# Kernel optimization log

Measured on AMD Instinct MI355X. Metric: run time of the kernel, lower is better.

The kernel has to match this reference:

```python
import jax, jax.numpy as jnp
import numpy as np

RESOLUTION = 128


def _bin_mask():
    # [4, 2] bool: corner i, dim d -> True if corner uses floor coord in dim d
    neigs = jnp.arange(4, dtype=jnp.int32)[:, None]
    dims = jnp.arange(2, dtype=jnp.int32)[None, :]
    return (neigs & (1 << dims)) == 0


def setup_inputs() -> dict:
    key = jax.random.key(0)
    k1, k2 = jax.random.split(key)
    batch = 65536
    res, map_num, feat_dim = RESOLUTION, 128, 8
    inputs = jax.random.uniform(k1, (batch, 2), dtype=jnp.float32)
    # xavier_uniform over [res^2, map_num*feat_dim]
    fan_in, fan_out = res * res, map_num * feat_dim
    bound = float(np.sqrt(6.0 / (fan_in + fan_out)))
    embeddings = jax.random.uniform(k2, (res * res, map_num * feat_dim),
                                    dtype=jnp.float32, minval=-bound, maxval=bound)
    return {"inputs": inputs, "embeddings": embeddings}


def reference(inputs, embeddings):
    res = RESOLUTION
    bin_mask = _bin_mask()                      # [4, 2]
    x = inputs * (res - 1)                      # [B, 2]
    xi = jnp.floor(x).astype(jnp.int32)         # [B, 2]
    xf = x - jax.lax.stop_gradient(jnp.floor(x))  # fractional part, grads flow via x
    xi = xi[:, None, :]                         # [B, 1, 2]
    xf = xf[:, None, :]                         # [B, 1, 2]
    neigs = jnp.where(bin_mask, xi, xi + 1)     # [B, 4, 2]
    ids = neigs[..., 0] * res + neigs[..., 1]   # [B, 4]
    neigs_features = embeddings[ids]            # [B, 4, D] irregular gather
    weights = jnp.where(bin_mask, 1.0 - xf, xf) # [B, 4, 2]
    w = jnp.prod(weights, axis=-1, keepdims=True)  # [B, 4, 1]
    return jnp.sum(neigs_features * w, axis=-2)    # [B, D]
```

## Files before the change

kernel.cpp:

```cpp
#include <hip/hip_runtime.h>

#define RES   128
#define FEAT  1024
#define NBINS (RES * RES)

__global__ __launch_bounds__(256)
void hist_kernel(const float* __restrict__ inputs, unsigned* __restrict__ hist, int N)
{
    int p = blockIdx.x * 256 + threadIdx.x;
    if (p >= N) return;
    int i0 = (int)floorf(inputs[2 * p + 0] * (float)(RES - 1));
    int i1 = (int)floorf(inputs[2 * p + 1] * (float)(RES - 1));
    atomicAdd(&hist[i0 * RES + i1], 1u);
}

__global__ __launch_bounds__(256)
void scan_kernel(unsigned* __restrict__ hist)
{
    __shared__ unsigned part[256];
    int t = threadIdx.x;
    int base = t * 64;
    unsigned s = 0;
    for (int k = 0; k < 64; ++k) s += hist[base + k];
    part[t] = s;
    __syncthreads();
    if (t == 0) {
        unsigned run = 0;
        for (int i = 0; i < 256; ++i) { unsigned v = part[i]; part[i] = run; run += v; }
    }
    __syncthreads();
    unsigned run = part[t];
    for (int k = 0; k < 64; ++k) { unsigned v = hist[base + k]; hist[base + k] = run; run += v; }
}

__global__ __launch_bounds__(256)
void scatter_kernel(const float* __restrict__ inputs, unsigned* __restrict__ hist,
                    unsigned* __restrict__ order, int N)
{
    int p = blockIdx.x * 256 + threadIdx.x;
    if (p >= N) return;
    int i0 = (int)floorf(inputs[2 * p + 0] * (float)(RES - 1));
    int i1 = (int)floorf(inputs[2 * p + 1] * (float)(RES - 1));
    unsigned pos = atomicAdd(&hist[i0 * RES + i1], 1u);
    order[pos] = (unsigned)p;
}

__global__ __launch_bounds__(256)
void DenseMap_sorted_kernel(const float* __restrict__ inputs,
                            const float* __restrict__ emb,
                            const unsigned* __restrict__ order,
                            float* __restrict__ out,
                            int N, int chunk)
{
    const int b = blockIdx.x;
    const int c = threadIdx.x;
    const int g = (chunk > 0) ? ((b & 7) * chunk + (b >> 3)) : b;

#pragma unroll
    for (int j = 0; j < 4; ++j) {
        const int s = g * 4 + j;
        if (s >= N) break;
        const int p = (int)order[s];

        const float x0 = inputs[2 * p + 0] * (float)(RES - 1);
        const float x1 = inputs[2 * p + 1] * (float)(RES - 1);
        const float f0 = floorf(x0);
        const float f1 = floorf(x1);
        const int   i0 = (int)f0;
        const int   i1 = (int)f1;
        const float xf0 = x0 - f0;
        const float xf1 = x1 - f1;

        const float w00 = (1.0f - xf0) * (1.0f - xf1);
        const float w01 = (1.0f - xf0) * xf1;
        const float w10 = xf0 * (1.0f - xf1);
        const float w11 = xf0 * xf1;

        const long base = (long)(i0 * RES + i1) * FEAT;
        const float4 a = ((const float4*)(emb + base))[c];
        const float4 bb = ((const float4*)(emb + base + FEAT))[c];
        const float4 gg = ((const float4*)(emb + base + (long)RES * FEAT))[c];
        const float4 h = ((const float4*)(emb + base + (long)RES * FEAT + FEAT))[c];

        float4 r;
        r.x = a.x * w00 + bb.x * w01 + gg.x * w10 + h.x * w11;
        r.y = a.y * w00 + bb.y * w01 + gg.y * w10 + h.y * w11;
        r.z = a.z * w00 + bb.z * w01 + gg.z * w10 + h.z * w11;
        r.w = a.w * w00 + bb.w * w01 + gg.w * w10 + h.w * w11;

        ((float4*)(out + (long)p * FEAT))[c] = r;
    }
}

__global__ __launch_bounds__(256)
void DenseMap_fallback_kernel(const float* __restrict__ inputs,
                              const float* __restrict__ emb,
                              float* __restrict__ out)
{
    const int p = blockIdx.x;
    const int c = threadIdx.x;

    const float x0 = inputs[2 * p + 0] * (float)(RES - 1);
    const float x1 = inputs[2 * p + 1] * (float)(RES - 1);
    const float f0 = floorf(x0);
    const float f1 = floorf(x1);
    const int   i0 = (int)f0;
    const int   i1 = (int)f1;
    const float xf0 = x0 - f0;
    const float xf1 = x1 - f1;

    const float w00 = (1.0f - xf0) * (1.0f - xf1);
    const float w01 = (1.0f - xf0) * xf1;
    const float w10 = xf0 * (1.0f - xf1);
    const float w11 = xf0 * xf1;

    const long base = (long)(i0 * RES + i1) * FEAT;
    const float4 a = ((const float4*)(emb + base))[c];
    const float4 b = ((const float4*)(emb + base + FEAT))[c];
    const float4 g = ((const float4*)(emb + base + (long)RES * FEAT))[c];
    const float4 h = ((const float4*)(emb + base + (long)RES * FEAT + FEAT))[c];

    float4 r;
    r.x = a.x * w00 + b.x * w01 + g.x * w10 + h.x * w11;
    r.y = a.y * w00 + b.y * w01 + g.y * w10 + h.y * w11;
    r.z = a.z * w00 + b.z * w01 + g.z * w10 + h.z * w11;
    r.w = a.w * w00 + b.w * w01 + g.w * w10 + h.w * w11;

    ((float4*)(out + (long)p * FEAT))[c] = r;
}

extern "C" void kernel_launch(void* const* d_in, const int* in_sizes, int n_in,
                              void* d_out, int out_size, void* d_ws, size_t ws_size,
                              hipStream_t stream)
{
    const float* inputs = (const float*)d_in[0];
    const float* emb    = (const float*)d_in[1];
    float*       out    = (float*)d_out;

    const int N = in_sizes[0] / 2;
    const size_t need = (size_t)(NBINS + N) * sizeof(unsigned);

    if (ws_size >= need) {
        unsigned* hist  = (unsigned*)d_ws;
        unsigned* order = hist + NBINS;

        hipMemsetAsync(hist, 0, NBINS * sizeof(unsigned), stream);
        hist_kernel<<<(N + 255) / 256, 256, 0, stream>>>(inputs, hist, N);
        scan_kernel<<<1, 256, 0, stream>>>(hist);
        scatter_kernel<<<(N + 255) / 256, 256, 0, stream>>>(inputs, hist, order, N);

        const int G = (N + 3) / 4;
        const int chunk = (G % 8 == 0) ? (G / 8) : 0;
        DenseMap_sorted_kernel<<<G, 256, 0, stream>>>(inputs, emb, order, out, N, chunk);
    } else {
        DenseMap_fallback_kernel<<<N, 256, 0, stream>>>(inputs, emb, out);
    }
}
```

Baseline: 389.2 us.

## Process one grid cell per block, reusing corner embeddings across its points

Replaces the per-point sorted kernel with a per-cell kernel that loads the four corner embedding rows once and applies them to every point falling in that cell. Point indices and coordinates are staged through shared memory, and outputs use nontemporal stores. This removes redundant embedding reads across points sharing a cell. It adds barriers per batch and can leave blocks with uneven amounts of work.

Measured after the change: 347.7 us. -10.7%, faster.

```diff
diff --git a/kernel.cpp b/kernel.cpp
--- a/kernel.cpp
+++ b/kernel.cpp
@@ -4,13 +4,16 @@
 #define FEAT  1024
 #define NBINS (RES * RES)
 
+typedef float nfloat4 __attribute__((ext_vector_type(4)));
+
 __global__ __launch_bounds__(256)
 void hist_kernel(const float* __restrict__ inputs, unsigned* __restrict__ hist, int N)
 {
     int p = blockIdx.x * 256 + threadIdx.x;
     if (p >= N) return;
-    int i0 = (int)floorf(inputs[2 * p + 0] * (float)(RES - 1));
-    int i1 = (int)floorf(inputs[2 * p + 1] * (float)(RES - 1));
+    const float2 uv = ((const float2*)inputs)[p];
+    int i0 = (int)floorf(uv.x * (float)(RES - 1));
+    int i1 = (int)floorf(uv.y * (float)(RES - 1));
     atomicAdd(&hist[i0 * RES + i1], 1u);
 }
 
@@ -39,56 +42,73 @@
 {
     int p = blockIdx.x * 256 + threadIdx.x;
     if (p >= N) return;
-    int i0 = (int)floorf(inputs[2 * p + 0] * (float)(RES - 1));
-    int i1 = (int)floorf(inputs[2 * p + 1] * (float)(RES - 1));
+    const float2 uv = ((const float2*)inputs)[p];
+    int i0 = (int)floorf(uv.x * (float)(RES - 1));
+    int i1 = (int)floorf(uv.y * (float)(RES - 1));
     unsigned pos = atomicAdd(&hist[i0 * RES + i1], 1u);
     order[pos] = (unsigned)p;
 }
 
 __global__ __launch_bounds__(256)
-void DenseMap_sorted_kernel(const float* __restrict__ inputs,
-                            const float* __restrict__ emb,
-                            const unsigned* __restrict__ order,
-                            float* __restrict__ out,
-                            int N, int chunk)
+void DenseMap_cell_kernel(const float* __restrict__ inputs,
+                          const float* __restrict__ emb,
+                          const unsigned* __restrict__ hist,
+                          const unsigned* __restrict__ order,
+                          float* __restrict__ out,
+                          int chunk)
 {
-    const int b = blockIdx.x;
-    const int c = threadIdx.x;
-    const int g = (chunk > 0) ? ((b & 7) * chunk + (b >> 3)) : b;
+    const int b    = blockIdx.x;
+    const int cell = (chunk > 0) ? ((b & 7) * chunk + (b >> 3)) : b;
+    const int c    = threadIdx.x;
 
-#pragma unroll
-    for (int j = 0; j < 4; ++j) {
-        const int s = g * 4 + j;
-        if (s >= N) break;
-        const int p = (int)order[s];
+    const unsigned start = (cell == 0) ? 0u : hist[cell - 1];
+    const unsigned end   = hist[cell];
+    if (start == end) return;
 
-        const float x0 = inputs[2 * p + 0] * (float)(RES - 1);
-        const float x1 = inputs[2 * p + 1] * (float)(RES - 1);
-        const float f0 = floorf(x0);
-        const float f1 = floorf(x1);
-        const int   i0 = (int)f0;
-        const int   i1 = (int)f1;
-        const float xf0 = x0 - f0;
-        const float xf1 = x1 - f1;
+    const int i0 = cell >> 7;
+    const int i1 = cell & (RES - 1);
 
-        const float w00 = (1.0f - xf0) * (1.0f - xf1);
-        const float w01 = (1.0f - xf0) * xf1;
-        const float w10 = xf0 * (1.0f - xf1);
-        const float w11 = xf0 * xf1;
+    const long base = (long)cell * FEAT;
+    const float4 r00 = ((const float4*)(emb + base))[c];
+    const float4 r01 = ((const float4*)(emb + base + FEAT))[c];
+    const float4 r10 = ((const float4*)(emb + base + (long)RES * FEAT))[c];
+    const float4 r11 = ((const float4*)(emb + base + (long)RES * FEAT + FEAT))[c];
 
-        const long base = (long)(i0 * RES + i1) * FEAT;
-        const float4 a = ((const float4*)(emb + base))[c];
-        const float4 bb = ((const float4*)(emb + base + FEAT))[c];
-        const float4 gg = ((const float4*)(emb + base + (long)RES * FEAT))[c];
-        const float4 h = ((const float4*)(emb + base + (long)RES * FEAT + FEAT))[c];
+    __shared__ unsigned sp[256];
+    __shared__ float    sx0[256];
+    __shared__ float    sx1[256];
 
-        float4 r;
-        r.x = a.x * w00 + bb.x * w01 + gg.x * w10 + h.x * w11;
-        r.y = a.y * w00 + bb.y * w01 + gg.y * w10 + h.y * w11;
-        r.z = a.z * w00 + bb.z * w01 + gg.z * w10 + h.z * w11;
-        r.w = a.w * w00 + bb.w * w01 + gg.w * w10 + h.w * w11;
+    for (unsigned cb = start; cb < end; cb += 256u) {
+        const int cnt = (int)min(end - cb, 256u);
+        if (c < cnt) {
+            const unsigned p  = order[cb + c];
+            const float2   uv = ((const float2*)inputs)[p];
+            sp[c]  = p;
+            sx0[c] = uv.x;
+            sx1[c] = uv.y;
+        }
+        __syncthreads();
 
-        ((float4*)(out + (long)p * FEAT))[c] = r;
+        for (int j = 0; j < cnt; ++j) {
+            const float x0  = sx0[j] * (float)(RES - 1);
+            const float x1  = sx1[j] * (float)(RES - 1);
+            const float xf0 = x0 - (float)i0;
+            const float xf1 = x1 - (float)i1;
+
+            const float w00 = (1.0f - xf0) * (1.0f - xf1);
+            const float w01 = (1.0f - xf0) * xf1;
+            const float w10 = xf0 * (1.0f - xf1);
+            const float w11 = xf0 * xf1;
+
+            nfloat4 r;
+            r.x = r00.x * w00 + r01.x * w01 + r10.x * w10 + r11.x * w11;
+            r.y = r00.y * w00 + r01.y * w01 + r10.y * w10 + r11.y * w11;
+            r.z = r00.z * w00 + r01.z * w01 + r10.z * w10 + r11.z * w11;
+            r.w = r00.w * w00 + r01.w * w01 + r10.w * w10 + r11.w * w11;
+
+            __builtin_nontemporal_store(r, ((nfloat4*)(out + (long)sp[j] * FEAT)) + c);
+        }
+        __syncthreads();
     }
 }
 
@@ -144,14 +164,13 @@
         unsigned* hist  = (unsigned*)d_ws;
         unsigned* order = hist + NBINS;
 
-        hipMemsetAsync(hist, 0, NBINS * sizeof(unsigned), stream);
+        (void)hipMemsetAsync(hist, 0, NBINS * sizeof(unsigned), stream);
         hist_kernel<<<(N + 255) / 256, 256, 0, stream>>>(inputs, hist, N);
         scan_kernel<<<1, 256, 0, stream>>>(hist);
         scatter_kernel<<<(N + 255) / 256, 256, 0, stream>>>(inputs, hist, order, N);
 
-        const int G = (N + 3) / 4;
-        const int chunk = (G % 8 == 0) ? (G / 8) : 0;
-        DenseMap_sorted_kernel<<<G, 256, 0, stream>>>(inputs, emb, order, out, N, chunk);
+        const int chunk = NBINS / 8;
+        DenseMap_cell_kernel<<<NBINS, 256, 0, stream>>>(inputs, emb, hist, order, out, chunk);
     } else {
         DenseMap_fallback_kernel<<<N, 256, 0, stream>>>(inputs, emb, out);
     }
```
